# Performance work log

Hardware: AMD Instinct MI355X
Metric: run time of the kernel (lower is better)

Reference implementation:

```python
import jax, jax.numpy as jnp
import numpy as np

B, C, N = 4, 16, 128
H_SET = 128   # set_layers[0]
D_OUT = 128   # channel_layers[0]


def setup_inputs() -> dict:
    key = jax.random.key(0)
    ks = jax.random.split(key, 7)
    x = jax.random.normal(ks[0], (B, C, N, N), dtype=jnp.float32)
    # phi: Linear(4 -> 128), ReLU, Linear(128 -> 2)
    W1 = jax.random.normal(ks[1], (H_SET, 4), dtype=jnp.float32) * 0.5
    b1 = jax.random.normal(ks[2], (H_SET,), dtype=jnp.float32) * 0.05
    W2 = jax.random.normal(ks[3], (2, H_SET), dtype=jnp.float32) * 0.1
    b2 = jax.random.normal(ks[4], (2,), dtype=jnp.float32) * 0.05
    # channel_fc: Conv2d(C -> 128, kernel 1) + ReLU  (1x1 conv == channel matmul)
    Wc = jax.random.normal(ks[5], (D_OUT, C), dtype=jnp.float32) * (1.0 / np.sqrt(C))
    bc = jax.random.normal(ks[6], (D_OUT,), dtype=jnp.float32) * 0.05
    return {"x": x, "W1": W1, "b1": b1, "W2": W2, "b2": b2, "Wc": Wc, "bc": bc}


def reference(x, W1, b1, W2, b2, Wc, bc):
    Bx, Cx, n, _ = x.shape
    ii = jnp.arange(n - 1)
    jj = jnp.arange(n)
    # group element g = i*n + j selects index pair (p, q) = (j, (j+i+1) mod n)
    p = jnp.broadcast_to(jj[None, :], (n - 1, n)).reshape(-1)        # (G,)
    q = ((jj[None, :] + ii[:, None] + 1) % n).reshape(-1)            # (G,)
    idx = jnp.stack([p, q], axis=-1)                                 # (G, 2)
    # gather 2x2 blocks: block[b,c,g] = x[b,c][[p,q]][:, [p,q]]
    block = x[:, :, idx[:, :, None], idx[:, None, :]]                # (B,C,G,2,2)
    v = block.reshape(Bx, Cx, -1, 4)                                 # (B,C,G,4)
    # phi: tiny per-element MLP 4 -> H -> 2
    h = jax.nn.relu(v @ W1.T + b1) @ W2.T + b2                       # (B,C,G,2)
    # scatter: off-diagonal entries get h[..., 1] at (p, q) (indices unique)
    out = jnp.zeros((Bx, Cx, n, n), x.dtype).at[:, :, p, q].set(h[..., 1])
    # diagonal: diag[j] = sum_i h[:, :, i*n + j, 0]
    diag = h[..., 0].reshape(Bx, Cx, n - 1, n).sum(axis=2)           # (B,C,n)
    ar = jnp.arange(n)
    out = out.at[:, :, ar, ar].add(diag)
    # coeff: 1 off-diagonal, 1/(n-1) on diagonal
    eye = jnp.eye(n, dtype=x.dtype)
    coeff = (1.0 - eye) + eye * (1.0 / (n - 1))
    out = out * coeff
    # channel_fc: 1x1 conv + ReLU
    y = jax.nn.relu(jnp.einsum('bcnm,dc->bdnm', out, Wc) + bc[None, :, None, None])
    return y
```

## Files before the change

### kernel.cpp

```cpp
#include <hip/hip_runtime.h>

#define NN 128
#define CCH 16
#define BBATCH 4
#define GP 4
#define HID 128

__global__ __launch_bounds__(128) void k1_mlp(
    const float* __restrict__ x, const float* __restrict__ W1,
    const float* __restrict__ b1, const float* __restrict__ W2,
    const float* __restrict__ b2, float* __restrict__ out)
{
    __shared__ float4 w1s[HID];
    __shared__ float4 wbs[HID];
    __shared__ float partial[2][GP];

    const int t = threadIdx.x;
    w1s[t] = reinterpret_cast<const float4*>(W1)[t];
    wbs[t] = make_float4(b1[t], W2[t], W2[HID + t], 0.f);

    const int bid = blockIdx.x;
    const int pg = bid & (NN / GP - 1);
    const int c  = (bid / (NN / GP)) & (CCH - 1);
    const int b  = bid / ((NN / GP) * CCH);
    const int p0 = pg * GP;

    const float* xm = x + (size_t)(b * CCH + c) * NN * NN;
    const int q = t;

    const float x_qq = xm[q * NN + q];
    const float4 colv = *reinterpret_cast<const float4*>(&xm[q * NN + p0]);
    float x_qp[GP] = { colv.x, colv.y, colv.z, colv.w };
    float x_pq[GP], x_pp[GP];
    #pragma unroll
    for (int i = 0; i < GP; ++i) {
        const int p = p0 + i;
        x_pp[i] = xm[p * NN + p];
        x_pq[i] = xm[p * NN + q];
    }
    const float bb0 = b2[0], bb1 = b2[1];
    float h0[GP], h1[GP];
    #pragma unroll
    for (int i = 0; i < GP; ++i) { h0[i] = bb0; h1[i] = bb1; }

    __syncthreads();

    #pragma unroll 8
    for (int k = 0; k < HID; ++k) {
        const float4 w  = w1s[k];
        const float4 wb = wbs[k];
        #pragma unroll
        for (int i = 0; i < GP; ++i) {
            float hd = fmaf(w.x, x_pp[i], wb.x);
            hd = fmaf(w.y, x_pq[i], hd);
            hd = fmaf(w.z, x_qp[i], hd);
            hd = fmaf(w.w, x_qq, hd);
            hd = fmaxf(hd, 0.f);
            h0[i] = fmaf(wb.y, hd, h0[i]);
            h1[i] = fmaf(wb.z, hd, h1[i]);
        }
    }

    float* orow = out + (size_t)(b * CCH + c) * NN * NN;
    #pragma unroll
    for (int i = 0; i < GP; ++i) {
        const int p = p0 + i;
        if (q != p) orow[p * NN + q] = h1[i];
        if (q == p) h0[i] = 0.f;
    }

    #pragma unroll
    for (int i = 0; i < GP; ++i) {
        float v = h0[i];
        for (int off = 32; off > 0; off >>= 1)
            v += __shfl_down(v, off, 64);
        if ((t & 63) == 0) partial[t >> 6][i] = v;
    }
    __syncthreads();
    if (t < GP) {
        const int p = p0 + t;
        orow[p * NN + p] = (partial[0][t] + partial[1][t]) * (1.0f / 127.0f);
    }
}

__global__ __launch_bounds__(256) void k2_conv(
    const float* __restrict__ outm, const float* __restrict__ Wc,
    const float* __restrict__ bc, float* __restrict__ y)
{
    __shared__ float s_out[CCH][NN];
    __shared__ float wcs[128][CCH];
    __shared__ float bcs[128];

    const int t = threadIdx.x;
    const int bid = blockIdx.x;
    const int nrow = bid & (NN - 1);
    const int b = bid / NN;

    #pragma unroll
    for (int i = 0; i < 8; ++i) {
        const int idx = t + i * 256;
        reinterpret_cast<float*>(wcs)[idx] = Wc[idx];
    }
    if (t < 128) bcs[t] = bc[t];

    const float* obase = outm + ((size_t)(b * CCH) * NN + nrow) * NN;
    #pragma unroll
    for (int i = 0; i < 8; ++i) {
        const int idx = t + i * 256;
        const int c = idx >> 7, m = idx & 127;
        s_out[c][m] = obase[(size_t)c * NN * NN + m];
    }
    __syncthreads();

    const int m0 = (t & 31) * 4;
    const int dgrp = t >> 5;

    float4 r[CCH];
    #pragma unroll
    for (int c2 = 0; c2 < CCH; ++c2)
        r[c2] = *reinterpret_cast<const float4*>(&s_out[c2][m0]);

    float* ybase = y + ((size_t)b * 128 * NN + nrow) * NN;
    #pragma unroll
    for (int dd = 0; dd < 16; ++dd) {
        const int d = dgrp * 16 + dd;
        const float bcv = bcs[d];
        float4 acc = make_float4(bcv, bcv, bcv, bcv);
        #pragma unroll
        for (int c2 = 0; c2 < CCH; ++c2) {
            const float wv = wcs[d][c2];
            acc.x = fmaf(wv, r[c2].x, acc.x);
            acc.y = fmaf(wv, r[c2].y, acc.y);
            acc.z = fmaf(wv, r[c2].z, acc.z);
            acc.w = fmaf(wv, r[c2].w, acc.w);
        }
        acc.x = fmaxf(acc.x, 0.f);
        acc.y = fmaxf(acc.y, 0.f);
        acc.z = fmaxf(acc.z, 0.f);
        acc.w = fmaxf(acc.w, 0.f);
        *reinterpret_cast<float4*>(&ybase[(size_t)d * NN * NN + m0]) = acc;
    }
}

extern "C" void kernel_launch(void* const* d_in, const int* in_sizes, int n_in,
                              void* d_out, int out_size, void* d_ws, size_t ws_size,
                              hipStream_t stream) {
    const float* x  = (const float*)d_in[0];
    const float* W1 = (const float*)d_in[1];
    const float* b1 = (const float*)d_in[2];
    const float* W2 = (const float*)d_in[3];
    const float* b2 = (const float*)d_in[4];
    const float* Wc = (const float*)d_in[5];
    const float* bc = (const float*)d_in[6];
    float* y  = (float*)d_out;
    float* ws = (float*)d_ws;

    dim3 g1(BBATCH * CCH * (NN / GP));
    k1_mlp<<<g1, 128, 0, stream>>>(x, W1, b1, W2, b2, ws);

    dim3 g2(BBATCH * NN);
    k2_conv<<<g2, 256, 0, stream>>>(ws, Wc, bc, y);
}
```

Before: 39.80 us.

## Fuse set-MLP and channel 1x1 conv into a single kernel via shared memory

Merges the per-pair MLP kernel and the channel-mixing conv kernel into one launch. Each block of 512 threads handles two rows p for all 16 channels of one batch and keeps the intermediate rows in shared memory. It then runs the 16->128 channel matmul with ReLU directly from that buffer. This removes the global workspace write and read of the intermediate tensor and one kernel launch. The cost is a much smaller grid (256 blocks), more registers per thread and lower occupancy during the MLP phase.

Measured after the change: 39.70 us. No clear change (-0.3%).

```diff
diff --git a/kernel.cpp b/kernel.cpp
--- a/kernel.cpp
+++ b/kernel.cpp
@@ -2,143 +2,146 @@
 
 #define NN 128
 #define CCH 16
-#define BBATCH 4
-#define GP 4
+#define BB 4
+#define GP 2
 #define HID 128
+#define DOUT 128
 
-__global__ __launch_bounds__(128) void k1_mlp(
+__global__ __launch_bounds__(512, 2) void fused_rey(
     const float* __restrict__ x, const float* __restrict__ W1,
     const float* __restrict__ b1, const float* __restrict__ W2,
-    const float* __restrict__ b2, float* __restrict__ out)
+    const float* __restrict__ b2, const float* __restrict__ Wc,
+    const float* __restrict__ bc, float* __restrict__ y)
 {
     __shared__ float4 w1s[HID];
     __shared__ float4 wbs[HID];
-    __shared__ float partial[2][GP];
+    __shared__ float  wcs[DOUT][CCH];
+    __shared__ float  bcs[DOUT];
+    __shared__ float  s_out[CCH][GP][NN];
+    __shared__ float  s_part[8][4][GP];
 
-    const int t = threadIdx.x;
-    w1s[t] = reinterpret_cast<const float4*>(W1)[t];
-    wbs[t] = make_float4(b1[t], W2[t], W2[HID + t], 0.f);
+    const int t   = threadIdx.x;
+    const int bid = blockIdx.x;
+    const int pg  = bid & 63;
+    const int b   = bid >> 6;
+    const int p0  = pg * GP;
+    const int q   = t & 127;
+    const int cq  = t >> 7;
 
-    const int bid = blockIdx.x;
-    const int pg = bid & (NN / GP - 1);
-    const int c  = (bid / (NN / GP)) & (CCH - 1);
-    const int b  = bid / ((NN / GP) * CCH);
-    const int p0 = pg * GP;
+    if (t < HID) {
+        w1s[t] = reinterpret_cast<const float4*>(W1)[t];
+        wbs[t] = make_float4(b1[t], W2[t], W2[HID + t], 0.f);
+        bcs[t] = bc[t];
+    }
+    reinterpret_cast<float4*>(wcs)[t] = reinterpret_cast<const float4*>(Wc)[t];
 
-    const float* xm = x + (size_t)(b * CCH + c) * NN * NN;
-    const int q = t;
-
-    const float x_qq = xm[q * NN + q];
-    const float4 colv = *reinterpret_cast<const float4*>(&xm[q * NN + p0]);
-    float x_qp[GP] = { colv.x, colv.y, colv.z, colv.w };
-    float x_pq[GP], x_pp[GP];
+    const float bb0 = b2[0], bb1 = b2[1];
+    float x_pp[4][GP], x_pq[4][GP], x_qp[4][GP], x_qq[4];
     #pragma unroll
-    for (int i = 0; i < GP; ++i) {
-        const int p = p0 + i;
-        x_pp[i] = xm[p * NN + p];
-        x_pq[i] = xm[p * NN + q];
+    for (int j = 0; j < 4; ++j) {
+        const int c = cq + 4 * j;
+        const float* xm = x + ((size_t)(b * CCH + c) << 14);
+        x_qq[j] = xm[q * (NN + 1)];
+        const float2 qp = *reinterpret_cast<const float2*>(&xm[q * NN + p0]);
+        x_qp[j][0] = qp.x; x_qp[j][1] = qp.y;
+        #pragma unroll
+        for (int pp = 0; pp < GP; ++pp) {
+            x_pp[j][pp] = xm[(p0 + pp) * (NN + 1)];
+            x_pq[j][pp] = xm[(p0 + pp) * NN + q];
+        }
     }
-    const float bb0 = b2[0], bb1 = b2[1];
-    float h0[GP], h1[GP];
+    float h0[4][GP], h1[4][GP];
     #pragma unroll
-    for (int i = 0; i < GP; ++i) { h0[i] = bb0; h1[i] = bb1; }
+    for (int j = 0; j < 4; ++j)
+        #pragma unroll
+        for (int pp = 0; pp < GP; ++pp) { h0[j][pp] = bb0; h1[j][pp] = bb1; }
 
     __syncthreads();
 
-    #pragma unroll 8
+    #pragma unroll 4
     for (int k = 0; k < HID; ++k) {
         const float4 w  = w1s[k];
         const float4 wb = wbs[k];
         #pragma unroll
-        for (int i = 0; i < GP; ++i) {
-            float hd = fmaf(w.x, x_pp[i], wb.x);
-            hd = fmaf(w.y, x_pq[i], hd);
-            hd = fmaf(w.z, x_qp[i], hd);
-            hd = fmaf(w.w, x_qq, hd);
-            hd = fmaxf(hd, 0.f);
-            h0[i] = fmaf(wb.y, hd, h0[i]);
-            h1[i] = fmaf(wb.z, hd, h1[i]);
+        for (int j = 0; j < 4; ++j) {
+            const float s = fmaf(w.w, x_qq[j], wb.x);
+            #pragma unroll
+            for (int pp = 0; pp < GP; ++pp) {
+                float hd = fmaf(w.x, x_pp[j][pp], s);
+                hd = fmaf(w.y, x_pq[j][pp], hd);
+                hd = fmaf(w.z, x_qp[j][pp], hd);
+                hd = fmaxf(hd, 0.f);
+                h0[j][pp] = fmaf(wb.y, hd, h0[j][pp]);
+                h1[j][pp] = fmaf(wb.z, hd, h1[j][pp]);
+            }
         }
     }
 
-    float* orow = out + (size_t)(b * CCH + c) * NN * NN;
     #pragma unroll
-    for (int i = 0; i < GP; ++i) {
-        const int p = p0 + i;
-        if (q != p) orow[p * NN + q] = h1[i];
-        if (q == p) h0[i] = 0.f;
+    for (int j = 0; j < 4; ++j) {
+        const int c = cq + 4 * j;
+        #pragma unroll
+        for (int pp = 0; pp < GP; ++pp) {
+            s_out[c][pp][q] = h1[j][pp];
+            if (q == p0 + pp) h0[j][pp] = 0.f;
+        }
     }
 
+    const int wv = t >> 6;
     #pragma unroll
-    for (int i = 0; i < GP; ++i) {
-        float v = h0[i];
-        for (int off = 32; off > 0; off >>= 1)
-            v += __shfl_down(v, off, 64);
-        if ((t & 63) == 0) partial[t >> 6][i] = v;
-    }
+    for (int j = 0; j < 4; ++j)
+        #pragma unroll
+        for (int pp = 0; pp < GP; ++pp) {
+            float v = h0[j][pp];
+            for (int off = 32; off > 0; off >>= 1)
+                v += __shfl_down(v, off, 64);
+            if ((t & 63) == 0) s_part[wv][j][pp] = v;
+        }
     __syncthreads();
-    if (t < GP) {
-        const int p = p0 + t;
-        orow[p * NN + p] = (partial[0][t] + partial[1][t]) * (1.0f / 127.0f);
-    }
-}
-
-__global__ __launch_bounds__(256) void k2_conv(
-    const float* __restrict__ outm, const float* __restrict__ Wc,
-    const float* __restrict__ bc, float* __restrict__ y)
-{
-    __shared__ float s_out[CCH][NN];
-    __shared__ float wcs[128][CCH];
-    __shared__ float bcs[128];
-
-    const int t = threadIdx.x;
-    const int bid = blockIdx.x;
-    const int nrow = bid & (NN - 1);
-    const int b = bid / NN;
-
-    #pragma unroll
-    for (int i = 0; i < 8; ++i) {
-        const int idx = t + i * 256;
-        reinterpret_cast<float*>(wcs)[idx] = Wc[idx];
-    }
-    if (t < 128) bcs[t] = bc[t];
-
-    const float* obase = outm + ((size_t)(b * CCH) * NN + nrow) * NN;
-    #pragma unroll
-    for (int i = 0; i < 8; ++i) {
-        const int idx = t + i * 256;
-        const int c = idx >> 7, m = idx & 127;
-        s_out[c][m] = obase[(size_t)c * NN * NN + m];
+    if (t < 32) {
+        const int cq2 = t >> 3, j2 = (t >> 1) & 3, pp2 = t & 1;
+        const int c2 = cq2 + 4 * j2;
+        const float v = (s_part[cq2 * 2][j2][pp2] + s_part[cq2 * 2 + 1][j2][pp2])
+                        * (1.0f / (NN - 1));
+        s_out[c2][pp2][p0 + pp2] = v;
     }
     __syncthreads();
 
-    const int m0 = (t & 31) * 4;
+    const int m0   = (t & 31) * 4;
     const int dgrp = t >> 5;
-
-    float4 r[CCH];
     #pragma unroll
-    for (int c2 = 0; c2 < CCH; ++c2)
-        r[c2] = *reinterpret_cast<const float4*>(&s_out[c2][m0]);
-
-    float* ybase = y + ((size_t)b * 128 * NN + nrow) * NN;
-    #pragma unroll
-    for (int dd = 0; dd < 16; ++dd) {
-        const int d = dgrp * 16 + dd;
-        const float bcv = bcs[d];
-        float4 acc = make_float4(bcv, bcv, bcv, bcv);
+    for (int pp = 0; pp < GP; ++pp) {
+        float4 r[CCH];
         #pragma unroll
-        for (int c2 = 0; c2 < CCH; ++c2) {
-            const float wv = wcs[d][c2];
-            acc.x = fmaf(wv, r[c2].x, acc.x);
-            acc.y = fmaf(wv, r[c2].y, acc.y);
-            acc.z = fmaf(wv, r[c2].z, acc.z);
-            acc.w = fmaf(wv, r[c2].w, acc.w);
+        for (int c = 0; c < CCH; ++c)
+            r[c] = *reinterpret_cast<const float4*>(&s_out[c][pp][m0]);
+        #pragma unroll
+        for (int dd = 0; dd < 8; ++dd) {
+            const int d = dgrp * 8 + dd;
+            const float4 wr0 = reinterpret_cast<const float4*>(&wcs[d][0])[0];
+            const float4 wr1 = reinterpret_cast<const float4*>(&wcs[d][0])[1];
+            const float4 wr2 = reinterpret_cast<const float4*>(&wcs[d][0])[2];
+            const float4 wr3 = reinterpret_cast<const float4*>(&wcs[d][0])[3];
+            const float wv16[16] = { wr0.x, wr0.y, wr0.z, wr0.w,
+                                     wr1.x, wr1.y, wr1.z, wr1.w,
+                                     wr2.x, wr2.y, wr2.z, wr2.w,
+                                     wr3.x, wr3.y, wr3.z, wr3.w };
+            const float bcv = bcs[d];
+            float4 acc = make_float4(bcv, bcv, bcv, bcv);
+            #pragma unroll
+            for (int c = 0; c < CCH; ++c) {
+                acc.x = fmaf(wv16[c], r[c].x, acc.x);
+                acc.y = fmaf(wv16[c], r[c].y, acc.y);
+                acc.z = fmaf(wv16[c], r[c].z, acc.z);
+                acc.w = fmaf(wv16[c], r[c].w, acc.w);
+            }
+            acc.x = fmaxf(acc.x, 0.f);
+            acc.y = fmaxf(acc.y, 0.f);
+            acc.z = fmaxf(acc.z, 0.f);
+            acc.w = fmaxf(acc.w, 0.f);
+            float* yp = y + ((((size_t)(b * DOUT + d)) * NN + (p0 + pp)) * NN + m0);
+            *reinterpret_cast<float4*>(yp) = acc;
         }
-        acc.x = fmaxf(acc.x, 0.f);
-        acc.y = fmaxf(acc.y, 0.f);
-        acc.z = fmaxf(acc.z, 0.f);
-        acc.w = fmaxf(acc.w, 0.f);
-        *reinterpret_cast<float4*>(&ybase[(size_t)d * NN * NN + m0]) = acc;
     }
 }
 
@@ -152,12 +155,8 @@
     const float* b2 = (const float*)d_in[4];
     const float* Wc = (const float*)d_in[5];
     const float* bc = (const float*)d_in[6];
-    float* y  = (float*)d_out;
-    float* ws = (float*)d_ws;
+    float* y = (float*)d_out;
 
-    dim3 g1(BBATCH * CCH * (NN / GP));
-    k1_mlp<<<g1, 128, 0, stream>>>(x, W1, b1, W2, b2, ws);
-
-    dim3 g2(BBATCH * NN);
-    k2_conv<<<g2, 256, 0, stream>>>(ws, Wc, bc, y);
+    dim3 grid(BB * (NN / GP));
+    fused_rey<<<grid, 512, 0, stream>>>(x, W1, b1, W2, b2, Wc, bc, y);
 }
```
